# Kernel tuning notes

Hardware: AMD Instinct MI355X
Metric: run time of the kernel (lower is better)

## Reference

```python
import jax, jax.numpy as jnp
import numpy as np

RATIOS = np.array([0.5, 1.0, 2.0], np.float32)
SCALES = np.array([8.0, 16.0, 32.0], np.float32)
IMAGE_SIZE = 1920.0
UPPER, LOWER = 0.4, 0.1
NPOS_MAX, NNEG_MAX = 128, 60   # sample_num=256 -> bg_num = min(60, 256-npos) = 60
BETA = 0.1
EPS = 1e-6


def make_anchors(H, W, stride):
    # K = len(RATIOS)*len(SCALES) anchors per grid cell, sizes stride*scale, aspect per ratio
    ws = (stride * SCALES[None, :] * np.sqrt(1.0 / RATIOS[:, None])).reshape(-1)  # [K]
    hs = (stride * SCALES[None, :] * np.sqrt(RATIOS[:, None])).reshape(-1)        # [K]
    cx = (np.arange(W, dtype=np.float32) + 0.5) * stride
    cy = (np.arange(H, dtype=np.float32) + 0.5) * stride
    cxg, cyg = np.meshgrid(cx, cy)  # [H, W]
    a = np.stack([cxg[..., None] - ws / 2, cyg[..., None] - hs / 2,
                  cxg[..., None] + ws / 2, cyg[..., None] + hs / 2], axis=-1)  # [H, W, K, 4]
    return jnp.asarray(a, jnp.float32)


def pairwise_iou(b, g):
    # b: [A, 4], g: [M, 4] -> [A, M]
    ab = jnp.maximum(b[:, 2] - b[:, 0], 0.0) * jnp.maximum(b[:, 3] - b[:, 1], 0.0)
    ag = jnp.maximum(g[:, 2] - g[:, 0], 0.0) * jnp.maximum(g[:, 3] - g[:, 1], 0.0)
    x1 = jnp.maximum(b[:, None, 0], g[None, :, 0])
    y1 = jnp.maximum(b[:, None, 1], g[None, :, 1])
    x2 = jnp.minimum(b[:, None, 2], g[None, :, 2])
    y2 = jnp.minimum(b[:, None, 3], g[None, :, 3])
    inter = jnp.maximum(x2 - x1, 0.0) * jnp.maximum(y2 - y1, 0.0)
    return inter / (ab[:, None] + ag[None, :] - inter + EPS)


def encode(box, anchor):
    # standard (tx, ty, tw, th) box encoding relative to anchor
    aw = anchor[:, 2] - anchor[:, 0]; ah = anchor[:, 3] - anchor[:, 1]
    acx = anchor[:, 0] + 0.5 * aw; acy = anchor[:, 1] + 0.5 * ah
    bw = jnp.maximum(box[:, 2] - box[:, 0], EPS); bh = jnp.maximum(box[:, 3] - box[:, 1], EPS)
    bcx = box[:, 0] + 0.5 * bw; bcy = box[:, 1] + 0.5 * bh
    return jnp.stack([(bcx - acx) / aw, (bcy - acy) / ah,
                      jnp.log(bw / aw), jnp.log(bh / ah)], axis=-1)


def smooth_l1(d):
    ad = jnp.abs(d)
    return jnp.where(ad < BETA, 0.5 * d * d / BETA, ad - 0.5 * BETA)


def per_image(regions, cls, gt, key, anchors_flat, n_norm):
    iou = pairwise_iou(regions, gt)                       # [A, M]
    best = iou.max(axis=1)
    arg = iou.argmax(axis=1).astype(jnp.int32)
    # match(): >= upper -> gt index (positive), < lower -> NEGATIVE(-1), else ignore(-2)
    matches = jnp.where(best >= UPPER, arg, jnp.where(best < LOWER, -1, -2))
    kp, kn = jax.random.split(key)
    # randperm-style sampling without replacement: top_k over random scores on masked anchors
    pos_score = jnp.where(matches >= 0, jax.random.uniform(kp, matches.shape), -1.0)
    pv, pidx = jax.lax.top_k(pos_score, NPOS_MAX)
    pvalid = (pv > 0.0).astype(jnp.float32)               # npos = min(num_pos, 128)
    neg_score = jnp.where(matches == -1, jax.random.uniform(kn, matches.shape), -1.0)
    nv, nidx = jax.lax.top_k(neg_score, NNEG_MAX)
    nvalid = (nv > 0.0).astype(jnp.float32)
    npos = pvalid.sum(); nneg = nvalid.sum()
    lp = cls[pidx]; ln = cls[nidx]
    # BCEWithLogits(mean): label 1 -> softplus(-x), label 0 -> softplus(x)
    bce = jnp.sum(jax.nn.softplus(-lp) * pvalid) + jnp.sum(jax.nn.softplus(ln) * nvalid)
    denom = jnp.maximum(npos + nneg, 1.0)
    cls_loss = bce / denom
    gt_sel = gt[jnp.clip(matches[pidx], 0, gt.shape[0] - 1)]
    anc = anchors_flat[pidx]
    tp = encode(regions[pidx], anc)
    tg = encode(gt_sel, anc)
    l1 = smooth_l1(tp - tg).sum(-1)                       # [NPOS_MAX]
    bbox_loss = jnp.sum(l1 * pvalid) / (jnp.maximum(npos, 1.0) * n_norm)
    pred_mean = (jnp.sum(lp * pvalid) + jnp.sum(ln * nvalid)) / denom
    return cls_loss, bbox_loss, npos, nneg, pred_mean


def reference(cls_scores, bbox_deltas, gt_boxes):
    N, K, H, W = cls_scores.shape
    stride = round(IMAGE_SIZE / W)
    anc = make_anchors(H, W, stride)                      # [H, W, K, 4]
    deltas = bbox_deltas.transpose(0, 2, 3, 1).reshape(N, H, W, K, 4)
    # regions = anchors + deltas, cross_boundary(remove=False) -> clip to image
    regions = jnp.clip(anc[None] + deltas, 0.0, IMAGE_SIZE).reshape(N, -1, 4)
    cls = cls_scores.transpose(0, 2, 3, 1).reshape(N, -1)
    keys = jax.random.split(jax.random.key(42), N)
    cl, bl, fg, bg, pm = jax.vmap(per_image, in_axes=(0, 0, 0, 0, None, None))(
        regions, cls, gt_boxes, keys, anc.reshape(-1, 4), float(N))
    return (cl.sum(), bl.sum(), bg.sum(), fg.sum(), pm[-1])


def setup_inputs():
    key = jax.random.key(0)
    k1, k2, k3, k4 = jax.random.split(key, 4)
    N, K, H, W, M = 8, 9, 120, 120, 64
    cls_scores = jax.random.normal(k1, (N, K, H, W), jnp.float32)
    bbox_deltas = jax.random.normal(k2, (N, 4 * K, H, W), jnp.float32) * 4.0
    xy = jax.random.uniform(k3, (N, M, 2), jnp.float32) * 1500.0
    wh = jax.random.uniform(k4, (N, M, 2), jnp.float32) * 360.0 + 40.0
    gt_boxes = jnp.concatenate([xy, xy + wh], axis=-1)    # valid [x1,y1,x2,y2] in-image
    return {"cls_scores": cls_scores, "bbox_deltas": bbox_deltas, "gt_boxes": gt_boxes}
```

## Files before the change

kernel.cpp:

```cpp
#include <hip/hip_runtime.h>
#include <stdint.h>

#define N_IMG 8
#define K_ANC 9
#define HW_G  14400
#define W_G   120
#define A_TOT 129600
#define M_GT  64
#define NBIN  1024
#define CAP   2048
#define WIN_TOT 2025
#define WPB   4
#define NSUB2 32

#define POISON_U32 0xAAAAAAAAu

static constexpr size_t OFF_PHIST = 0;
static constexpr size_t OFF_NHIST = 32768;
static constexpr size_t OFF_CNT   = 65536;
static constexpr size_t OFF_THR   = 65600;
static constexpr size_t OFF_DONE  = 65856;
static constexpr size_t OFF_ACC   = 65920;
static constexpr size_t OFF_ENT   = 67584;
static constexpr size_t OFF_BND   = OFF_ENT + 4ull * N_IMG * A_TOT;

__device__ __forceinline__ uint32_t rotl32(uint32_t v, int r) {
  return (v << r) | (v >> (32 - r));
}

__device__ void tf2x32(uint32_t k0, uint32_t k1, uint32_t x0, uint32_t x1,
                       uint32_t& o0, uint32_t& o1) {
  uint32_t ks2 = 0x1BD11BDAu ^ k0 ^ k1;
  x0 += k0; x1 += k1;
#define TF_R(r) { x0 += x1; x1 = rotl32(x1, r); x1 ^= x0; }
  TF_R(13) TF_R(15) TF_R(26) TF_R(6)
  x0 += k1; x1 += ks2 + 1u;
  TF_R(17) TF_R(29) TF_R(16) TF_R(24)
  x0 += ks2; x1 += k0 + 2u;
  TF_R(13) TF_R(15) TF_R(26) TF_R(6)
  x0 += k0; x1 += k1 + 3u;
  TF_R(17) TF_R(29) TF_R(16) TF_R(24)
  x0 += k1; x1 += ks2 + 4u;
  TF_R(13) TF_R(15) TF_R(26) TF_R(6)
  x0 += ks2; x1 += k0 + 5u;
#undef TF_R
  o0 = x0; o1 = x1;
}

constexpr uint64_t tf_c(uint32_t k0, uint32_t k1, uint32_t x0, uint32_t x1) {
  const int R[20] = {13,15,26,6,17,29,16,24,13,15,26,6,17,29,16,24,13,15,26,6};
  uint32_t ks[3] = {k0, k1, 0x1BD11BDAu ^ k0 ^ k1};
  x0 += k0; x1 += k1;
  for (int r = 0; r < 20; ++r) {
    x0 += x1; x1 = (x1 << R[r]) | (x1 >> (32 - R[r])); x1 ^= x0;
    if ((r & 3) == 3) {
      int d = r / 4 + 1;
      x0 += ks[d % 3]; x1 += ks[(d + 1) % 3] + (uint32_t)d;
    }
  }
  return ((uint64_t)x0 << 32) | x1;
}

struct KeyTab { uint32_t v[N_IMG][4]; };
constexpr KeyTab make_keys() {
  KeyTab K{};
  for (int n = 0; n < N_IMG; ++n) {
    uint64_t f = tf_c(0u, 42u, 0u, (uint32_t)n);
    uint32_t i0 = (uint32_t)(f >> 32), i1 = (uint32_t)f;
    uint64_t p = tf_c(i0, i1, 0u, 0u);
    uint64_t q = tf_c(i0, i1, 0u, 1u);
    K.v[n][0] = (uint32_t)(p >> 32); K.v[n][1] = (uint32_t)p;
    K.v[n][2] = (uint32_t)(q >> 32); K.v[n][3] = (uint32_t)q;
  }
  return K;
}
__constant__ KeyTab KEYS = make_keys();

__device__ void acc_pos(int n, int l, int m, const float* __restrict__ cls,
                        const float* __restrict__ del, const float* __restrict__ gt,
                        float& sp, float& pr, float& l1s) {
  int k = l / HW_G, hw = l - k * HW_G;
  const float scales[3] = {8.f, 16.f, 32.f};
  const float ratios[3] = {0.5f, 1.f, 2.f};
  float sc = scales[k % 3], rt = ratios[k / 3];
  float wsz = (16.f * sc) * sqrtf(1.f / rt);
  float hsz = (16.f * sc) * sqrtf(rt);
  int w = hw % W_G, h = hw / W_G;
  float cx = ((float)w + 0.5f) * 16.f, cy = ((float)h + 0.5f) * 16.f;
  float ax1 = cx - wsz * 0.5f, ay1 = cy - hsz * 0.5f;
  float ax2 = cx + wsz * 0.5f, ay2 = cy + hsz * 0.5f;
  int base = (n * 36 + k * 4) * HW_G + hw;
  float rx1 = fminf(fmaxf(ax1 + del[base], 0.f), 1920.f);
  float ry1 = fminf(fmaxf(ay1 + del[base + HW_G], 0.f), 1920.f);
  float rx2 = fminf(fmaxf(ax2 + del[base + 2 * HW_G], 0.f), 1920.f);
  float ry2 = fminf(fmaxf(ay2 + del[base + 3 * HW_G], 0.f), 1920.f);
  float L = cls[n * A_TOT + l];
  sp += fmaxf(-L, 0.f) + log1pf(expf(-fabsf(L)));
  pr += L;
  const float* g = gt + (n * M_GT + m) * 4;
  float aw = ax2 - ax1, ah = ay2 - ay1;
  float acx = ax1 + 0.5f * aw, acy = ay1 + 0.5f * ah;
  float bw = fmaxf(rx2 - rx1, 1e-6f), bh = fmaxf(ry2 - ry1, 1e-6f);
  float bcx = rx1 + 0.5f * bw, bcy = ry1 + 0.5f * bh;
  float gw = fmaxf(g[2] - g[0], 1e-6f), gh = fmaxf(g[3] - g[1], 1e-6f);
  float gcx = g[0] + 0.5f * gw, gcy = g[1] + 0.5f * gh;
  float dd[4];
  dd[0] = (bcx - acx) / aw - (gcx - acx) / aw;
  dd[1] = (bcy - acy) / ah - (gcy - acy) / ah;
  dd[2] = logf(bw / aw) - logf(gw / aw);
  dd[3] = logf(bh / ah) - logf(gh / ah);
  float t = 0.f;
  for (int i = 0; i < 4; ++i) {
    float ad = fabsf(dd[i]);
    t += (ad < 0.1f) ? (0.5f * dd[i] * dd[i] / 0.1f) : (ad - 0.05f);
  }
  l1s += t;
}

__device__ void acc_neg(int n, int l, const float* __restrict__ cls,
                        float& sp, float& pr) {
  float L = cls[n * A_TOT + l];
  sp += fmaxf(L, 0.f) + log1pf(expf(-fabsf(L)));
  pr += L;
}

__device__ void reduce3_atomic(float sp, float pr, float l1, float* accf, int n,
                               int tid) {
  __shared__ float swv[3][4];
  float v0 = sp, v1 = pr, v2 = l1;
  for (int off = 32; off > 0; off >>= 1) {
    v0 += __shfl_down(v0, off); v1 += __shfl_down(v1, off); v2 += __shfl_down(v2, off);
  }
  int wv = tid >> 6, ln = tid & 63;
  if (ln == 0) { swv[0][wv] = v0; swv[1][wv] = v1; swv[2][wv] = v2; }
  __syncthreads();
  if (tid == 0) {
    atomicAdd(&accf[n * 48 + 0],  swv[0][0] + swv[0][1] + swv[0][2] + swv[0][3]);
    atomicAdd(&accf[n * 48 + 16], swv[1][0] + swv[1][1] + swv[1][2] + swv[1][3]);
    atomicAdd(&accf[n * 48 + 32], swv[2][0] + swv[2][1] + swv[2][2] + swv[2][3]);
  }
  __syncthreads();
}

__global__ __launch_bounds__(256) void k_match(
    const float* __restrict__ del, const float* __restrict__ gt, uint8_t* ws) {
  const int n = blockIdx.y;
  const int tid = threadIdx.x;
  const int wid = tid >> 6, ln = tid & 63;
  const int win = blockIdx.x * WPB + wid;
  __shared__ float4 cbox[WPB][M_GT];
  __shared__ float car[WPB][M_GT];
  __shared__ int cidx[WPB][M_GT];
  if (win >= WIN_TOT) return;
  const int k = win / 225;
  const int hw = (win - k * 225) * 64 + ln;

  float4 g4 = reinterpret_cast<const float4*>(gt)[n * M_GT + ln];

  const float scales[3] = {8.f, 16.f, 32.f};
  const float ratios[3] = {0.5f, 1.f, 2.f};
  float sc = scales[k % 3], rt = ratios[k / 3];
  float wsz = (16.f * sc) * sqrtf(1.f / rt);
  float hsz = (16.f * sc) * sqrtf(rt);
  int w = hw % W_G, h = hw / W_G;
  float cx = ((float)w + 0.5f) * 16.f, cy = ((float)h + 0.5f) * 16.f;
  float ax1 = cx - wsz * 0.5f, ay1 = cy - hsz * 0.5f;
  float ax2 = cx + wsz * 0.5f, ay2 = cy + hsz * 0.5f;
  const float* dp = del + (size_t)(n * 36 + k * 4) * HW_G + hw;
  float rx1 = fminf(fmaxf(ax1 + dp[0], 0.f), 1920.f);
  float ry1 = fminf(fmaxf(ay1 + dp[HW_G], 0.f), 1920.f);
  float rx2 = fminf(fmaxf(ax2 + dp[2 * HW_G], 0.f), 1920.f);
  float ry2 = fminf(fmaxf(ay2 + dp[3 * HW_G], 0.f), 1920.f);
  float ab = fmaxf(rx2 - rx1, 0.f) * fmaxf(ry2 - ry1, 0.f);

  float xmn = rx1, xmx = rx2, ymn = ry1, ymx = ry2;
  for (int off = 32; off > 0; off >>= 1) {
    xmn = fminf(xmn, __shfl_xor(xmn, off));
    xmx = fmaxf(xmx, __shfl_xor(xmx, off));
    ymn = fminf(ymn, __shfl_xor(ymn, off));
    ymx = fmaxf(ymx, __shfl_xor(ymx, off));
  }
  bool keep = (g4.x < xmx) && (g4.z > xmn) && (g4.y < ymx) && (g4.w > ymn);
  unsigned long long mk = __ballot(keep);
  int Mp = __popcll(mk);
  if (keep) {
    int pos = __popcll(mk & ((1ull << ln) - 1ull));
    cbox[wid][pos] = g4;
    car[wid][pos] = fmaxf(g4.z - g4.x, 0.f) * fmaxf(g4.w - g4.y, 0.f);
    cidx[wid][pos] = ln;
  }

  float ib = -1.f, ub = 1.f;
  int arg = 0;
  for (int j = 0; j < Mp; ++j) {
    float4 b = cbox[wid][j];
    float ga = car[wid][j];
    int oj = cidx[wid][j];
    float ix1 = fmaxf(rx1, b.x), iy1 = fmaxf(ry1, b.y);
    float ix2 = fminf(rx2, b.z), iy2 = fminf(ry2, b.w);
    float inter = fmaxf(ix2 - ix1, 0.f) * fmaxf(iy2 - iy1, 0.f);
    float u = ab + ga - inter + 1e-6f;
    bool gc = (inter * ub) > (ib * u);
    ib = gc ? inter : ib;
    ub = gc ? u : ub;
    arg = gc ? oj : arg;
  }
  float best = ib / ub;
  int m = (best >= 0.4f) ? arg : ((best < 0.1f) ? -1 : -2);

  uint32_t a32 = (uint32_t)(hw * 9 + k);
  uint32_t sk0 = (m >= 0) ? KEYS.v[n][0] : KEYS.v[n][2];
  uint32_t sk1 = (m >= 0) ? KEYS.v[n][1] : KEYS.v[n][3];
  uint32_t y0, y1;
  tf2x32(sk0, sk1, 0u, a32, y0, y1);
  uint32_t bits = (y0 ^ y1) >> 9;

  uint32_t e = 0u;
  if (bits) {
    if (m >= 0)       e = 0x80000000u | ((uint32_t)m << 23) | bits;
    else if (m == -1) e = bits;
  }
  ((uint32_t*)(ws + OFF_ENT))[(size_t)n * A_TOT + (size_t)k * HW_G + hw] = e;
  if (e) {
    uint32_t* hist = (uint32_t*)(ws + OFF_PHIST);
    uint32_t off = (e >> 31) ? 0u : (uint32_t)(N_IMG * NBIN);
    atomicAdd(&hist[off + n * NBIN + (bits >> 13)], 1u);
  }
}

__global__ __launch_bounds__(256) void k_scan_bound(
    const float* __restrict__ cls, const float* __restrict__ del,
    const float* __restrict__ gt, float* __restrict__ out, uint8_t* ws) {
  const int sub = blockIdx.x, n = blockIdx.y;
  const int tid = threadIdx.x;
  const uint32_t* hist = (const uint32_t*)(ws + OFF_PHIST);
  const uint32_t* ent = (const uint32_t*)(ws + OFF_ENT);
  uint32_t* cnt = (uint32_t*)(ws + OFF_CNT);
  int* thrg = (int*)(ws + OFF_THR);
  unsigned long long* bnd = (unsigned long long*)(ws + OFF_BND);
  float* accf = (float*)(ws + OFF_ACC);
  uint32_t* done_img = (uint32_t*)(ws + OFF_DONE);
  uint32_t* done_fin = (uint32_t*)(ws + OFF_DONE + 32);

  __shared__ unsigned long long sb[CAP];
  uint32_t* shist = (uint32_t*)sb;
  uint32_t* sfx = ((uint32_t*)sb) + 2 * NBIN;
  __shared__ int tbv[2][3];
  __shared__ int sLast, sFin;

  {
    const uint32_t* hp = hist + n * NBIN;
    const uint32_t* hn = hist + (size_t)N_IMG * NBIN + n * NBIN;
    for (int i = tid; i < NBIN; i += 256) {
      shist[i] = hp[i] - POISON_U32;
      shist[NBIN + i] = hn[i] - POISON_U32;
    }
  }
  __syncthreads();
  for (int wq = 0; wq < 2; ++wq) {
    const uint32_t* sh = shist + wq * NBIN;
    uint32_t cs = sh[tid * 4] + sh[tid * 4 + 1] + sh[tid * 4 + 2] + sh[tid * 4 + 3];
    sfx[tid] = cs;
    __syncthreads();
    for (int off = 1; off < 256; off <<= 1) {
      uint32_t v = (tid + off < 256) ? sfx[tid + off] : 0u;
      __syncthreads();
      sfx[tid] += v;
      __syncthreads();
    }
    const uint32_t kk = wq ? 60u : 128u;
    if (sfx[0] < kk) {
      if (tid == 0) { tbv[wq][0] = -1; tbv[wq][1] = 0; tbv[wq][2] = (int)sfx[0]; }
    } else {
      uint32_t above = (tid == 255) ? 0u : sfx[tid + 1];
      if (sfx[tid] >= kk && above < kk) {
        uint32_t c = above;
        for (int i = tid * 4 + 3;; --i) {
          uint32_t hc = sh[i];
          if (c + hc >= kk) {
            tbv[wq][0] = i; tbv[wq][1] = (int)(kk - c); tbv[wq][2] = (int)kk;
            break;
          }
          c += hc;
        }
      }
    }
    __syncthreads();
  }

  const int bBp = tbv[0][0], bBn = tbv[1][0];
  float sp = 0.f, pr = 0.f, l1 = 0.f;
  const uint32_t* en = ent + (size_t)n * A_TOT;
  for (int it = 0; it < 4; ++it) {
    int l0 = sub * 4096 + it * 1024 + tid * 4;
    if (l0 >= A_TOT) continue;
    uint4 e4 = *reinterpret_cast<const uint4*>(en + l0);
    uint32_t ev[4] = {e4.x, e4.y, e4.z, e4.w};
#pragma unroll
    for (int j = 0; j < 4; ++j) {
      uint32_t e = ev[j];
      if (!e) continue;
      bool isPos = (e >> 31) != 0u;
      int bB = isPos ? bBp : bBn;
      int l = l0 + j;
      uint32_t bits = e & 0x7FFFFFu;
      int bin = (int)(bits >> 13);
      if (bin > bB) {
        if (isPos) acc_pos(n, l, (int)((e >> 23) & 0x3Fu), cls, del, gt, sp, pr, l1);
        else       acc_neg(n, l, cls, sp, pr);
      } else if (bin == bB) {
        int wq = isPos ? 0 : 1;
        int i = (int)(atomicAdd(&cnt[n * 2 + wq], 1u) - POISON_U32);
        if (i < CAP) {
          int k = l / HW_G, hw = l - k * HW_G, a = hw * 9 + k;
          bnd[(size_t)(n * 2 + wq) * CAP + i] =
              ((unsigned long long)bits << 17) | (unsigned)(0x1FFFF - a);
        }
      }
    }
  }
  __threadfence();
  reduce3_atomic(sp, pr, l1, accf, n, tid);

  if (tid == 0)
    sLast = (atomicAdd(&done_img[n], 1u) == POISON_U32 + NSUB2 - 1u) ? 1 : 0;
  __syncthreads();
  if (!sLast) return;
  __threadfence();

  if (tid < 6) thrg[n * 6 + tid] = ((const int*)tbv)[tid];

  float sp2 = 0.f, pr2 = 0.f, l12 = 0.f;
  for (int wq = 0; wq < 2; ++wq) {
    int need = tbv[wq][1];
    if (need > 0) {
      __syncthreads();
      int m = min((int)(cnt[n * 2 + wq] - POISON_U32), CAP);
      const unsigned long long* bq = bnd + (size_t)(n * 2 + wq) * CAP;
      for (int i = tid; i < m; i += 256) sb[i] = bq[i];
      __syncthreads();
      for (int i = tid; i < m; i += 256) {
        unsigned long long key = sb[i];
        int rank = 0;
        for (int j = 0; j < m; ++j) rank += (sb[j] > key) ? 1 : 0;
        if (rank < need) {
          int a = 0x1FFFF - (int)(key & 0x1FFFFull);
          int k = a % 9, hw = a / 9;
          int l = k * HW_G + hw;
          if (wq == 0) {
            uint32_t e = ent[(size_t)n * A_TOT + l];
            acc_pos(n, l, (int)((e >> 23) & 0x3Fu), cls, del, gt, sp2, pr2, l12);
          } else {
            acc_neg(n, l, cls, sp2, pr2);
          }
        }
      }
      __syncthreads();
    }
  }
  reduce3_atomic(sp2, pr2, l12, accf, n, tid);

  __threadfence();
  if (tid == 0)
    sFin = (atomicAdd(done_fin, 1u) == POISON_U32 + N_IMG - 1u) ? 1 : 0;
  __syncthreads();
  if (!sFin) return;
  __threadfence();

  if (tid == 0) {
    const float PF = __uint_as_float(POISON_U32);
    const int* thrr = (const int*)(ws + OFF_THR);
    float c = 0.f, b = 0.f, fg = 0.f, bg = 0.f, pm = 0.f;
    for (int nn = 0; nn < N_IMG; ++nn) {
      float npos = (float)thrr[nn * 6 + 2];
      float nneg = (float)thrr[nn * 6 + 5];
      float denom = fmaxf(npos + nneg, 1.f);
      c += (accf[nn * 48 + 0] - PF) / denom;
      b += (accf[nn * 48 + 32] - PF) / (fmaxf(npos, 1.f) * 8.0f);
      fg += npos; bg += nneg;
      if (nn == N_IMG - 1) pm = (accf[nn * 48 + 16] - PF) / denom;
    }
    out[0] = c; out[1] = b; out[2] = bg; out[3] = fg; out[4] = pm;
  }
}

extern "C" void kernel_launch(void* const* d_in, const int* in_sizes, int n_in,
                              void* d_out, int out_size, void* d_ws, size_t ws_size,
                              hipStream_t stream) {
  (void)in_sizes; (void)n_in; (void)out_size; (void)ws_size;
  const float* cls = (const float*)d_in[0];
  const float* del = (const float*)d_in[1];
  const float* gt  = (const float*)d_in[2];
  float* out = (float*)d_out;
  uint8_t* ws = (uint8_t*)d_ws;

  hipLaunchKernelGGL(k_match, dim3((WIN_TOT + WPB - 1) / WPB, N_IMG), dim3(256),
                     0, stream, del, gt, ws);
  hipLaunchKernelGGL(k_scan_bound, dim3(NSUB2, N_IMG), dim3(256), 0, stream,
                     cls, del, gt, out, ws);
}
```

Measured before the change: 140.4 us.

## Tile match windows as 8x8 spatial patches and move histogram threshold scan into last match block

Each wave in the match kernel now covers an 8x8 spatial patch instead of a 64-wide row strip. The tighter window bounding box should let more ground-truth boxes be culled before the IoU loop. The per-image threshold search over the histograms moves out of every scan block and into the last finishing match block per image, using a wave-level shuffle scan, so the 2x1024-bin scan is no longer repeated in all scan blocks. The scan kernel also doubles its block count to halve per-block work. The costs are a completion counter and a threadfence in every match block, and the patch-shaped layout makes global loads of deltas and entry writes less coalesced.

```diff
diff --git a/kernel.cpp b/kernel.cpp
--- a/kernel.cpp
+++ b/kernel.cpp
@@ -11,7 +11,8 @@
 #define CAP   2048
 #define WIN_TOT 2025
 #define WPB   4
-#define NSUB2 32
+#define NBLK_M 507
+#define NSUB2 64
 
 #define POISON_U32 0xAAAAAAAAu
 
@@ -19,7 +20,9 @@
 static constexpr size_t OFF_NHIST = 32768;
 static constexpr size_t OFF_CNT   = 65536;
 static constexpr size_t OFF_THR   = 65600;
+static constexpr size_t OFF_DONE_M= 65792;
 static constexpr size_t OFF_DONE  = 65856;
+static constexpr size_t OFF_DONE_F= 65888;
 static constexpr size_t OFF_ACC   = 65920;
 static constexpr size_t OFF_ENT   = 67584;
 static constexpr size_t OFF_BND   = OFF_ENT + 4ull * N_IMG * A_TOT;
@@ -151,80 +154,126 @@
   __shared__ float4 cbox[WPB][M_GT];
   __shared__ float car[WPB][M_GT];
   __shared__ int cidx[WPB][M_GT];
-  if (win >= WIN_TOT) return;
-  const int k = win / 225;
-  const int hw = (win - k * 225) * 64 + ln;
-
-  float4 g4 = reinterpret_cast<const float4*>(gt)[n * M_GT + ln];
-
-  const float scales[3] = {8.f, 16.f, 32.f};
-  const float ratios[3] = {0.5f, 1.f, 2.f};
-  float sc = scales[k % 3], rt = ratios[k / 3];
-  float wsz = (16.f * sc) * sqrtf(1.f / rt);
-  float hsz = (16.f * sc) * sqrtf(rt);
-  int w = hw % W_G, h = hw / W_G;
-  float cx = ((float)w + 0.5f) * 16.f, cy = ((float)h + 0.5f) * 16.f;
-  float ax1 = cx - wsz * 0.5f, ay1 = cy - hsz * 0.5f;
-  float ax2 = cx + wsz * 0.5f, ay2 = cy + hsz * 0.5f;
-  const float* dp = del + (size_t)(n * 36 + k * 4) * HW_G + hw;
-  float rx1 = fminf(fmaxf(ax1 + dp[0], 0.f), 1920.f);
-  float ry1 = fminf(fmaxf(ay1 + dp[HW_G], 0.f), 1920.f);
-  float rx2 = fminf(fmaxf(ax2 + dp[2 * HW_G], 0.f), 1920.f);
-  float ry2 = fminf(fmaxf(ay2 + dp[3 * HW_G], 0.f), 1920.f);
-  float ab = fmaxf(rx2 - rx1, 0.f) * fmaxf(ry2 - ry1, 0.f);
-
-  float xmn = rx1, xmx = rx2, ymn = ry1, ymx = ry2;
-  for (int off = 32; off > 0; off >>= 1) {
-    xmn = fminf(xmn, __shfl_xor(xmn, off));
-    xmx = fmaxf(xmx, __shfl_xor(xmx, off));
-    ymn = fminf(ymn, __shfl_xor(ymn, off));
-    ymx = fmaxf(ymx, __shfl_xor(ymx, off));
-  }
-  bool keep = (g4.x < xmx) && (g4.z > xmn) && (g4.y < ymx) && (g4.w > ymn);
-  unsigned long long mk = __ballot(keep);
-  int Mp = __popcll(mk);
-  if (keep) {
-    int pos = __popcll(mk & ((1ull << ln) - 1ull));
-    cbox[wid][pos] = g4;
-    car[wid][pos] = fmaxf(g4.z - g4.x, 0.f) * fmaxf(g4.w - g4.y, 0.f);
-    cidx[wid][pos] = ln;
-  }
-
-  float ib = -1.f, ub = 1.f;
-  int arg = 0;
-  for (int j = 0; j < Mp; ++j) {
-    float4 b = cbox[wid][j];
-    float ga = car[wid][j];
-    int oj = cidx[wid][j];
-    float ix1 = fmaxf(rx1, b.x), iy1 = fmaxf(ry1, b.y);
-    float ix2 = fminf(rx2, b.z), iy2 = fminf(ry2, b.w);
-    float inter = fmaxf(ix2 - ix1, 0.f) * fmaxf(iy2 - iy1, 0.f);
-    float u = ab + ga - inter + 1e-6f;
-    bool gc = (inter * ub) > (ib * u);
-    ib = gc ? inter : ib;
-    ub = gc ? u : ub;
-    arg = gc ? oj : arg;
-  }
-  float best = ib / ub;
-  int m = (best >= 0.4f) ? arg : ((best < 0.1f) ? -1 : -2);
-
-  uint32_t a32 = (uint32_t)(hw * 9 + k);
-  uint32_t sk0 = (m >= 0) ? KEYS.v[n][0] : KEYS.v[n][2];
-  uint32_t sk1 = (m >= 0) ? KEYS.v[n][1] : KEYS.v[n][3];
-  uint32_t y0, y1;
-  tf2x32(sk0, sk1, 0u, a32, y0, y1);
-  uint32_t bits = (y0 ^ y1) >> 9;
-
-  uint32_t e = 0u;
-  if (bits) {
-    if (m >= 0)       e = 0x80000000u | ((uint32_t)m << 23) | bits;
-    else if (m == -1) e = bits;
-  }
-  ((uint32_t*)(ws + OFF_ENT))[(size_t)n * A_TOT + (size_t)k * HW_G + hw] = e;
-  if (e) {
-    uint32_t* hist = (uint32_t*)(ws + OFF_PHIST);
-    uint32_t off = (e >> 31) ? 0u : (uint32_t)(N_IMG * NBIN);
-    atomicAdd(&hist[off + n * NBIN + (bits >> 13)], 1u);
+  __shared__ int sLast;
+
+  if (win < WIN_TOT) {
+    const int k = win / 225;
+    const int t = win - k * 225;
+    const int ty = t / 15, tx = t - ty * 15;
+    const int h = ty * 8 + (ln >> 3), w = tx * 8 + (ln & 7);
+    const int hw = h * W_G + w;
+
+    float4 g4 = reinterpret_cast<const float4*>(gt)[n * M_GT + ln];
+
+    const float scales[3] = {8.f, 16.f, 32.f};
+    const float ratios[3] = {0.5f, 1.f, 2.f};
+    float sc = scales[k % 3], rt = ratios[k / 3];
+    float wsz = (16.f * sc) * sqrtf(1.f / rt);
+    float hsz = (16.f * sc) * sqrtf(rt);
+    float cx = ((float)w + 0.5f) * 16.f, cy = ((float)h + 0.5f) * 16.f;
+    float ax1 = cx - wsz * 0.5f, ay1 = cy - hsz * 0.5f;
+    float ax2 = cx + wsz * 0.5f, ay2 = cy + hsz * 0.5f;
+    const float* dp = del + (size_t)(n * 36 + k * 4) * HW_G + hw;
+    float rx1 = fminf(fmaxf(ax1 + dp[0], 0.f), 1920.f);
+    float ry1 = fminf(fmaxf(ay1 + dp[HW_G], 0.f), 1920.f);
+    float rx2 = fminf(fmaxf(ax2 + dp[2 * HW_G], 0.f), 1920.f);
+    float ry2 = fminf(fmaxf(ay2 + dp[3 * HW_G], 0.f), 1920.f);
+    float ab = fmaxf(rx2 - rx1, 0.f) * fmaxf(ry2 - ry1, 0.f);
+
+    float xmn = rx1, xmx = rx2, ymn = ry1, ymx = ry2;
+    for (int off = 32; off > 0; off >>= 1) {
+      xmn = fminf(xmn, __shfl_xor(xmn, off));
+      xmx = fmaxf(xmx, __shfl_xor(xmx, off));
+      ymn = fminf(ymn, __shfl_xor(ymn, off));
+      ymx = fmaxf(ymx, __shfl_xor(ymx, off));
+    }
+    bool keep = (g4.x < xmx) && (g4.z > xmn) && (g4.y < ymx) && (g4.w > ymn);
+    unsigned long long mk = __ballot(keep);
+    int Mp = __popcll(mk);
+    if (keep) {
+      int pos = __popcll(mk & ((1ull << ln) - 1ull));
+      cbox[wid][pos] = g4;
+      car[wid][pos] = fmaxf(g4.z - g4.x, 0.f) * fmaxf(g4.w - g4.y, 0.f);
+      cidx[wid][pos] = ln;
+    }
+
+    float ib = -1.f, ub = 1.f;
+    int arg = 0;
+    for (int j = 0; j < Mp; ++j) {
+      float4 b = cbox[wid][j];
+      float ga = car[wid][j];
+      int oj = cidx[wid][j];
+      float ix1 = fmaxf(rx1, b.x), iy1 = fmaxf(ry1, b.y);
+      float ix2 = fminf(rx2, b.z), iy2 = fminf(ry2, b.w);
+      float inter = fmaxf(ix2 - ix1, 0.f) * fmaxf(iy2 - iy1, 0.f);
+      float u = ab + ga - inter + 1e-6f;
+      bool gc = (inter * ub) > (ib * u);
+      ib = gc ? inter : ib;
+      ub = gc ? u : ub;
+      arg = gc ? oj : arg;
+    }
+    float best = ib / ub;
+    int m = (best >= 0.4f) ? arg : ((best < 0.1f) ? -1 : -2);
+
+    uint32_t a32 = (uint32_t)(hw * 9 + k);
+    uint32_t sk0 = (m >= 0) ? KEYS.v[n][0] : KEYS.v[n][2];
+    uint32_t sk1 = (m >= 0) ? KEYS.v[n][1] : KEYS.v[n][3];
+    uint32_t y0, y1;
+    tf2x32(sk0, sk1, 0u, a32, y0, y1);
+    uint32_t bits = (y0 ^ y1) >> 9;
+
+    uint32_t e = 0u;
+    if (bits) {
+      if (m >= 0)       e = 0x80000000u | ((uint32_t)m << 23) | bits;
+      else if (m == -1) e = bits;
+    }
+    ((uint32_t*)(ws + OFF_ENT))[(size_t)n * A_TOT + (size_t)k * HW_G + hw] = e;
+    if (e) {
+      uint32_t* hist = (uint32_t*)(ws + OFF_PHIST);
+      uint32_t off = (e >> 31) ? 0u : (uint32_t)(N_IMG * NBIN);
+      atomicAdd(&hist[off + n * NBIN + (bits >> 13)], 1u);
+    }
+  }
+
+  __syncthreads();
+  if (tid == 0) {
+    __threadfence();
+    uint32_t* dm = (uint32_t*)(ws + OFF_DONE_M);
+    sLast = (atomicAdd(&dm[n], 1u) == POISON_U32 + (uint32_t)(NBLK_M - 1)) ? 1 : 0;
+  }
+  __syncthreads();
+  if (sLast && wid < 2) {
+    const int s = wid;
+    const volatile uint32_t* hb = (const volatile uint32_t*)(ws + OFF_PHIST) +
+                                  (s ? (size_t)N_IMG * NBIN : 0) + (size_t)n * NBIN;
+    uint32_t hv[16];
+    uint32_t ssum = 0u;
+#pragma unroll
+    for (int i = 0; i < 16; ++i) { hv[i] = hb[ln * 16 + i] - POISON_U32; ssum += hv[i]; }
+    uint32_t sfx = ssum;
+#pragma unroll
+    for (int off = 1; off < 64; off <<= 1) {
+      uint32_t v = __shfl_down(sfx, off);
+      sfx += (ln + off < 64) ? v : 0u;
+    }
+    uint32_t total = __shfl(sfx, 0);
+    uint32_t ab1 = __shfl_down(sfx, 1);
+    uint32_t above = (ln == 63) ? 0u : ab1;
+    const uint32_t kk = s ? 60u : 128u;
+    int* thr = (int*)(ws + OFF_THR) + n * 6 + s * 3;
+    if (total < kk) {
+      if (ln == 0) { thr[0] = -1; thr[1] = 0; thr[2] = (int)total; }
+    } else if (sfx >= kk && above < kk) {
+      uint32_t c = above;
+      for (int i = 15;; --i) {
+        uint32_t hc = hv[i];
+        if (c + hc >= kk) {
+          thr[0] = ln * 16 + i; thr[1] = (int)(kk - c); thr[2] = (int)kk;
+          break;
+        }
+        c += hc;
+      }
+    }
   }
 }
 
@@ -233,66 +282,23 @@
     const float* __restrict__ gt, float* __restrict__ out, uint8_t* ws) {
   const int sub = blockIdx.x, n = blockIdx.y;
   const int tid = threadIdx.x;
-  const uint32_t* hist = (const uint32_t*)(ws + OFF_PHIST);
   const uint32_t* ent = (const uint32_t*)(ws + OFF_ENT);
   uint32_t* cnt = (uint32_t*)(ws + OFF_CNT);
-  int* thrg = (int*)(ws + OFF_THR);
+  const int* thr = (const int*)(ws + OFF_THR) + n * 6;
   unsigned long long* bnd = (unsigned long long*)(ws + OFF_BND);
   float* accf = (float*)(ws + OFF_ACC);
   uint32_t* done_img = (uint32_t*)(ws + OFF_DONE);
-  uint32_t* done_fin = (uint32_t*)(ws + OFF_DONE + 32);
+  uint32_t* done_fin = (uint32_t*)(ws + OFF_DONE_F);
 
   __shared__ unsigned long long sb[CAP];
-  uint32_t* shist = (uint32_t*)sb;
-  uint32_t* sfx = ((uint32_t*)sb) + 2 * NBIN;
-  __shared__ int tbv[2][3];
   __shared__ int sLast, sFin;
 
-  {
-    const uint32_t* hp = hist + n * NBIN;
-    const uint32_t* hn = hist + (size_t)N_IMG * NBIN + n * NBIN;
-    for (int i = tid; i < NBIN; i += 256) {
-      shist[i] = hp[i] - POISON_U32;
-      shist[NBIN + i] = hn[i] - POISON_U32;
-    }
-  }
-  __syncthreads();
-  for (int wq = 0; wq < 2; ++wq) {
-    const uint32_t* sh = shist + wq * NBIN;
-    uint32_t cs = sh[tid * 4] + sh[tid * 4 + 1] + sh[tid * 4 + 2] + sh[tid * 4 + 3];
-    sfx[tid] = cs;
-    __syncthreads();
-    for (int off = 1; off < 256; off <<= 1) {
-      uint32_t v = (tid + off < 256) ? sfx[tid + off] : 0u;
-      __syncthreads();
-      sfx[tid] += v;
-      __syncthreads();
-    }
-    const uint32_t kk = wq ? 60u : 128u;
-    if (sfx[0] < kk) {
-      if (tid == 0) { tbv[wq][0] = -1; tbv[wq][1] = 0; tbv[wq][2] = (int)sfx[0]; }
-    } else {
-      uint32_t above = (tid == 255) ? 0u : sfx[tid + 1];
-      if (sfx[tid] >= kk && above < kk) {
-        uint32_t c = above;
-        for (int i = tid * 4 + 3;; --i) {
-          uint32_t hc = sh[i];
-          if (c + hc >= kk) {
-            tbv[wq][0] = i; tbv[wq][1] = (int)(kk - c); tbv[wq][2] = (int)kk;
-            break;
-          }
-          c += hc;
-        }
-      }
-    }
-    __syncthreads();
-  }
-
-  const int bBp = tbv[0][0], bBn = tbv[1][0];
+  const int bBp = thr[0], bBn = thr[3];
   float sp = 0.f, pr = 0.f, l1 = 0.f;
   const uint32_t* en = ent + (size_t)n * A_TOT;
-  for (int it = 0; it < 4; ++it) {
-    int l0 = sub * 4096 + it * 1024 + tid * 4;
+#pragma unroll
+  for (int it = 0; it < 2; ++it) {
+    int l0 = sub * 2048 + it * 1024 + tid * 4;
     if (l0 >= A_TOT) continue;
     uint4 e4 = *reinterpret_cast<const uint4*>(en + l0);
     uint32_t ev[4] = {e4.x, e4.y, e4.z, e4.w};
@@ -328,11 +334,9 @@
   if (!sLast) return;
   __threadfence();
 
-  if (tid < 6) thrg[n * 6 + tid] = ((const int*)tbv)[tid];
-
   float sp2 = 0.f, pr2 = 0.f, l12 = 0.f;
   for (int wq = 0; wq < 2; ++wq) {
-    int need = tbv[wq][1];
+    int need = thr[wq * 3 + 1];
     if (need > 0) {
       __syncthreads();
       int m = min((int)(cnt[n * 2 + wq] - POISON_U32), CAP);
@@ -394,8 +398,8 @@
   float* out = (float*)d_out;
   uint8_t* ws = (uint8_t*)d_ws;
 
-  hipLaunchKernelGGL(k_match, dim3((WIN_TOT + WPB - 1) / WPB, N_IMG), dim3(256),
-                     0, stream, del, gt, ws);
+  hipLaunchKernelGGL(k_match, dim3(NBLK_M, N_IMG), dim3(256), 0, stream,
+                     del, gt, ws);
   hipLaunchKernelGGL(k_scan_bound, dim3(NSUB2, N_IMG), dim3(256), 0, stream,
                      cls, del, gt, out, ws);
 }
```

Result: slower. 251.8 us (+79.3%).
